# Kernel tuning notes

Hardware: AMD Instinct MI355X
Metric: run time of the kernel (lower is better)

The kernel has to match this reference:

```python
import jax, jax.numpy as jnp
import numpy as np

N, D = 8192, 128
T = 0.0025   # threshold t
M = 0.5      # margin m
K = 16
EPS = 1e-12


def _l2norm(x):
    return x / jnp.sqrt(jnp.sum(x * x, axis=-1, keepdims=True) + EPS)


def setup_inputs() -> dict:
    key = jax.random.key(0)
    k1, k2 = jax.random.split(key)
    yi = jax.random.normal(k1, (N, D), dtype=jnp.float32)
    yi_t = jax.random.normal(k2, (N, D), dtype=jnp.float32)
    return {"yi": yi, "yi_t": yi_t}


def reference(yi, yi_t):
    yin = _l2norm(yi)      # normalized yi, [N, D]
    yit = _l2norm(yi_t)    # normalized yi_t, [N, D]

    # pairwise L2 distances among normalized yi via norm expansion (avoids [N,N,D])
    sq = jnp.sum(yin * yin, axis=-1)                          # [N]
    d2 = sq[:, None] + sq[None, :] - 2.0 * (yin @ yin.T)      # [N, N]
    dis = jnp.sqrt(jnp.maximum(d2, 0.0) + EPS)

    # K+1 smallest distances per row (index 0 is self: self-dist = sqrt(EPS))
    _, idx = jax.lax.top_k(-dis, K + 1)                       # [N, K+1]

    yj = yin[idx[:, 1:]]    # [N, K, D] K nearest neighbors (excluding self)
    yij = yin[idx[:, 1]]    # [N, D]    nearest neighbor

    dis_yij = 0.5 * jnp.sqrt(jnp.sum((yin[:, None, :] - yj) ** 2, axis=-1) + EPS)   # [N, K]
    dis_yi_tj = 0.5 * jnp.sqrt(jnp.sum((yit[:, None, :] - yj) ** 2, axis=-1) + EPS)  # [N, K]

    out1 = (dis_yij - dis_yi_tj) ** 2 - T
    e1 = jnp.sum(jnp.where(out1 > 0, out1, 0.0))

    dis_yi_yi_t = 0.5 * jnp.sqrt(jnp.sum((yin - yit) ** 2, axis=-1) + EPS)  # [N]
    dis_yi_yij = 0.5 * jnp.sqrt(jnp.sum((yin - yij) ** 2, axis=-1) + EPS)   # [N]

    out2 = dis_yi_yi_t + M - dis_yi_yij
    e2 = jnp.sum(jnp.where(out2 > 0, out2, 0.0))

    return (e1 + e2, e1, e2)
```

## Files before the change

### kernel.cpp

```cpp
#include <hip/hip_runtime.h>
#include <hip/hip_bf16.h>
#include <math.h>


#define NPTS 8192
#define DIM 128
#define KNB 16
#define CAP 192
static constexpr float TAU = 0.20f;
static constexpr float T_THR = 0.0025f;
static constexpr float MARGIN = 0.5f;
static constexpr float EPSF = 1e-12f;

typedef __bf16 bf16x8 __attribute__((ext_vector_type(8)));
typedef float f32x4 __attribute__((ext_vector_type(4)));
struct bf2 { __bf16 x, y; };

__device__ __forceinline__ float bf2f(unsigned short u) {
    union { unsigned u32; float f; } c;
    c.u32 = ((unsigned)u) << 16;
    return c.f;
}

__global__ __launch_bounds__(256) void k_norm(const float* __restrict__ yi,
                                              const float* __restrict__ yit,
                                              __bf16* __restrict__ yb,
                                              __bf16* __restrict__ ybt,
                                              float* __restrict__ dyt,
                                              int* __restrict__ cnt) {
    const int g = blockIdx.x * 256 + threadIdx.x;
    if (g < NPTS) cnt[g] = 0;
    const int wid = threadIdx.x >> 6;
    const int lane = threadIdx.x & 63;
    const int row = blockIdx.x * 4 + wid;

    float2 v1 = *(const float2*)(yi + (size_t)row * DIM + lane * 2);
    float2 v2 = *(const float2*)(yit + (size_t)row * DIM + lane * 2);
    float s1 = v1.x * v1.x + v1.y * v1.y;
    float s2 = v2.x * v2.x + v2.y * v2.y;
    #pragma unroll
    for (int o = 32; o; o >>= 1) {
        s1 += __shfl_xor(s1, o);
        s2 += __shfl_xor(s2, o);
    }
    const float r1 = 1.0f / sqrtf(s1 + EPSF);
    const float r2 = 1.0f / sqrtf(s2 + EPSF);
    const float ax = v1.x * r1, ay = v1.y * r1;
    const float bx = v2.x * r2, by = v2.y * r2;
    bf2 oa{(__bf16)ax, (__bf16)ay};
    bf2 ob{(__bf16)bx, (__bf16)by};
    *(bf2*)(yb + (size_t)row * DIM + lane * 2) = oa;
    *(bf2*)(ybt + (size_t)row * DIM + lane * 2) = ob;

    float dd = (ax - bx) * (ax - bx) + (ay - by) * (ay - by);
    #pragma unroll
    for (int o = 32; o; o >>= 1) dd += __shfl_xor(dd, o);
    if (lane == 0) dyt[row] = 0.5f * sqrtf(dd + EPSF);
}

__global__ __launch_bounds__(256, 4) void k_screen(const __bf16* __restrict__ yb,
                                                   int* __restrict__ cnt,
                                                   unsigned* __restrict__ bucket) {
    __shared__ unsigned bucket_l[256 * 32];
    const int tid = threadIdx.x;
    const int wid = tid >> 6;
    const int lane = tid & 63;
    const int c15 = lane & 15;
    const int hi = lane >> 4;
    const int rb = blockIdx.x >> 5;
    const int cs = blockIdx.x & 31;
    const int wrow0 = rb * 256 + wid * 64;
    const int col0 = cs * 256;

    bf16x8 A[4][4];
    #pragma unroll
    for (int rt = 0; rt < 4; ++rt)
        #pragma unroll
        for (int t = 0; t < 4; ++t)
            A[rt][t] = *(const bf16x8*)(yb + (size_t)(wrow0 + rt * 16 + c15) * DIM + t * 32 + hi * 8);

    int cntr[4] = {0, 0, 0, 0};

    #pragma unroll 2
    for (int tile = 0; tile < 16; ++tile) {
        const int jc = col0 + tile * 16 + c15;
        const __bf16* bp = yb + (size_t)jc * DIM + hi * 8;
        const bf16x8 B0 = *(const bf16x8*)(bp);
        const bf16x8 B1 = *(const bf16x8*)(bp + 32);
        const bf16x8 B2 = *(const bf16x8*)(bp + 64);
        const bf16x8 B3 = *(const bf16x8*)(bp + 96);

        f32x4 acc[4];
        #pragma unroll
        for (int rt = 0; rt < 4; ++rt) {
            f32x4 z = {0.0f, 0.0f, 0.0f, 0.0f};
            acc[rt] = __builtin_amdgcn_mfma_f32_16x16x32_bf16(B0, A[rt][0], z, 0, 0, 0);
            acc[rt] = __builtin_amdgcn_mfma_f32_16x16x32_bf16(B1, A[rt][1], acc[rt], 0, 0, 0);
            acc[rt] = __builtin_amdgcn_mfma_f32_16x16x32_bf16(B2, A[rt][2], acc[rt], 0, 0, 0);
            acc[rt] = __builtin_amdgcn_mfma_f32_16x16x32_bf16(B3, A[rt][3], acc[rt], 0, 0, 0);
        }

        const int cb = col0 + tile * 16 + (hi << 2);
        const unsigned kbase = (unsigned)(8191 - cb);
        #pragma unroll
        for (int rt = 0; rt < 4; ++rt) {
            unsigned* bl = &bucket_l[(wid * 64 + rt * 16 + c15) * 32 + hi * 8];
            #pragma unroll
            for (int r = 0; r < 4; ++r) {
                const float v = acc[rt][r];
                const bool h = v > TAU;
                const unsigned key =
                    (__float_as_uint(v) & 0xFFFFE000u) | (kbase - (unsigned)r);
                const int idx = min(cntr[rt], 7);
                if (h) bl[idx] = key;
                cntr[rt] += (int)h;
            }
        }
    }

    unsigned cpack = (unsigned)min(cntr[0], 8) | ((unsigned)min(cntr[1], 8) << 8) |
                     ((unsigned)min(cntr[2], 8) << 16) | ((unsigned)min(cntr[3], 8) << 24);
    asm volatile("s_waitcnt lgkmcnt(0)" ::: "memory");
    {
        const int rt = (tid >> 4) & 3;
        const int cl = tid & 15;
        int c[4], total = 0;
        #pragma unroll
        for (int h2 = 0; h2 < 4; ++h2) {
            unsigned cp = __shfl(cpack, h2 * 16 + cl);
            c[h2] = (int)((cp >> (rt * 8)) & 255u);
            total += c[h2];
        }
        if (total > 0) {
            const int grow = rb * 256 + tid;
            int p = atomicAdd(&cnt[grow], total);
            const unsigned* bl = &bucket_l[tid * 32];
            #pragma unroll
            for (int h2 = 0; h2 < 4; ++h2)
                for (int s = 0; s < c[h2]; ++s) {
                    if (p < CAP) bucket[(size_t)grow * CAP + p] = bl[h2 * 8 + s];
                    ++p;
                }
        }
    }
}

__global__ __launch_bounds__(256) void k_selloss(const __bf16* __restrict__ yb,
                                                 const __bf16* __restrict__ ybt,
                                                 const int* __restrict__ cnt,
                                                 const unsigned* __restrict__ bucketK,
                                                 const float* __restrict__ dyt,
                                                 float* __restrict__ e1row,
                                                 float* __restrict__ e2row) {
    __shared__ unsigned nbrk[4][KNB];
    const int wid = threadIdx.x >> 6;
    const int lane = threadIdx.x & 63;
    const int row = blockIdx.x * 4 + wid;

    const int cn = min(cnt[row], CAP);
    unsigned val[3];
    #pragma unroll
    for (int s = 0; s < 3; ++s) {
        const int p = s * 64 + lane;
        val[s] = (p < cn) ? bucketK[(size_t)row * CAP + p] : 0u;
    }

    unsigned prefix = 0u;
    int need = 17;
    #pragma unroll 1
    for (int b = 29; b >= 0; --b) {
        const unsigned cand = prefix | (1u << b);
        int c = 0;
        #pragma unroll
        for (int s = 0; s < 3; ++s)
            c += __popcll(__ballot(((val[s] ^ cand) >> b) == 0u));
        if (c >= need) prefix = cand;
        else need -= c;
    }

    bool sel[3];
    unsigned m1 = 0u;
    #pragma unroll
    for (int s = 0; s < 3; ++s) {
        const int jj = 8191 - (int)(val[s] & 0x1FFFu);
        sel[s] = (val[s] >= prefix) && (jj != row);
        if (sel[s] && val[s] > m1) m1 = val[s];
    }
    #pragma unroll
    for (int o = 32; o; o >>= 1) {
        unsigned ov = __shfl_xor(m1, o);
        m1 = ov > m1 ? ov : m1;
    }
    {
        const unsigned long long b0 = __ballot(sel[0]);
        const unsigned long long b1 = __ballot(sel[1]);
        const unsigned long long b2 = __ballot(sel[2]);
        const unsigned long long lt = ((unsigned long long)1 << lane) - 1;
        const int n0 = __popcll(b0), n1 = __popcll(b1);
        const int p0 = __popcll(b0 & lt);
        const int p1 = n0 + __popcll(b1 & lt);
        const int p2 = n0 + n1 + __popcll(b2 & lt);
        if (sel[0] && p0 < KNB) nbrk[wid][p0] = val[0];
        if (sel[1] && p1 < KNB) nbrk[wid][p1] = val[1];
        if (sel[2] && p2 < KNB) nbrk[wid][p2] = val[2];
    }

    const int n = lane >> 2;
    const int cch = lane & 3;
    const unsigned key = nbrk[wid][n];
    const int j = (8191 - (int)(key & 0x1FFFu)) & (NPTS - 1);
    const bf16x8* pj = (const bf16x8*)(yb + (size_t)j * DIM + cch * 32);
    const bf16x8* pi = (const bf16x8*)(ybt + (size_t)row * DIM + cch * 32);
    float dd = 0.0f;
    #pragma unroll
    for (int q = 0; q < 4; ++q) {
        bf16x8 a = pi[q], b = pj[q];
        #pragma unroll
        for (int e = 0; e < 8; ++e) {
            const float d = bf2f(((const unsigned short*)&a)[e]) -
                            bf2f(((const unsigned short*)&b)[e]);
            dd += d * d;
        }
    }
    #pragma unroll
    for (int o = 1; o <= 2; o <<= 1) dd += __shfl_xor(dd, o);

    const float dotk = __uint_as_float(key & 0xFFFFE000u);
    const float da = 0.5f * sqrtf(fmaxf(2.0f - 2.0f * dotk, 0.0f) + EPSF);
    const float db = 0.5f * sqrtf(dd + EPSF);
    float o1 = (da - db) * (da - db) - T_THR;
    o1 = (cch == 0) ? fmaxf(o1, 0.0f) : 0.0f;
    #pragma unroll
    for (int o = 4; o <= 32; o <<= 1) o1 += __shfl_xor(o1, o);

    if (lane == 0) {
        const float dot1 = __uint_as_float(m1 & 0xFFFFE000u);
        const float d0 = 0.5f * sqrtf(fmaxf(2.0f - 2.0f * dot1, 0.0f) + EPSF);
        e1row[row] = o1;
        e2row[row] = fmaxf(dyt[row] + MARGIN - d0, 0.0f);
    }
}

__global__ __launch_bounds__(1024) void k_red(const float* __restrict__ e1row,
                                              const float* __restrict__ e2row,
                                              float* __restrict__ out) {
    __shared__ float s1[1024], s2[1024];
    float a = 0.0f, b = 0.0f;
    for (int i = threadIdx.x; i < NPTS; i += 1024) {
        a += e1row[i];
        b += e2row[i];
    }
    s1[threadIdx.x] = a;
    s2[threadIdx.x] = b;
    __syncthreads();
    for (int st = 512; st; st >>= 1) {
        if (threadIdx.x < st) {
            s1[threadIdx.x] += s1[threadIdx.x + st];
            s2[threadIdx.x] += s2[threadIdx.x + st];
        }
        __syncthreads();
    }
    if (threadIdx.x == 0) {
        float e1 = s1[0], e2 = s2[0];
        out[0] = e1 + e2;
        out[1] = e1;
        out[2] = e2;
    }
}

extern "C" void kernel_launch(void* const* d_in, const int* in_sizes, int n_in,
                              void* d_out, int out_size, void* d_ws, size_t ws_size,
                              hipStream_t stream) {
    const float* yi = (const float*)d_in[0];
    const float* yit = (const float*)d_in[1];

    __bf16* yb = (__bf16*)d_ws;
    __bf16* ybt = yb + (size_t)NPTS * DIM;
    int* cnt = (int*)(ybt + (size_t)NPTS * DIM);
    unsigned* bucketK = (unsigned*)(cnt + NPTS);
    float* dyt = (float*)(bucketK + (size_t)NPTS * CAP);
    float* e1row = dyt + NPTS;
    float* e2row = e1row + NPTS;

    k_norm<<<NPTS / 4, 256, 0, stream>>>(yi, yit, yb, ybt, dyt, cnt);
    k_screen<<<1024, 256, 0, stream>>>(yb, cnt, bucketK);
    k_selloss<<<NPTS / 4, 256, 0, stream>>>(yb, ybt, cnt, bucketK, dyt, e1row, e2row);
    k_red<<<1, 1024, 0, stream>>>(e1row, e2row, (float*)d_out);
}
```

Baseline: 68.43 us.

## Halve screen tile rows per block to raise occupancy and shrink LDS buckets

The screening kernel now gives each wave 32 rows instead of 64 and launches twice as many blocks. It cuts the per-lane LDS bucket slots from 8 to 6 and requests 8 waves per EU. MFMA chains for the two row tiles are interleaved so independent work sits between dependent steps. The goal is to lower register and LDS pressure so more waves can hide load latency. In exchange, each B column tile is reloaded twice as often, and rows with more than 6 hits per 16-column segment lose more candidates, which could change the kNN selection.

```diff
diff --git a/kernel.cpp b/kernel.cpp
--- a/kernel.cpp
+++ b/kernel.cpp
@@ -7,6 +7,7 @@
 #define DIM 128
 #define KNB 16
 #define CAP 192
+#define SLOTS 6
 static constexpr float TAU = 0.20f;
 static constexpr float T_THR = 0.0025f;
 static constexpr float MARGIN = 0.5f;
@@ -58,10 +59,12 @@
     if (lane == 0) dyt[row] = 0.5f * sqrtf(dd + EPSF);
 }
 
-__global__ __launch_bounds__(256, 4) void k_screen(const __bf16* __restrict__ yb,
-                                                   int* __restrict__ cnt,
-                                                   unsigned* __restrict__ bucket) {
-    __shared__ unsigned bucket_l[256 * 32];
+__global__ __launch_bounds__(256)
+__attribute__((amdgpu_waves_per_eu(8)))
+void k_screen(const __bf16* __restrict__ yb,
+              int* __restrict__ cnt,
+              unsigned* __restrict__ bucket) {
+    __shared__ unsigned bucket_l[128 * 4 * SLOTS];
     const int tid = threadIdx.x;
     const int wid = tid >> 6;
     const int lane = tid & 63;
@@ -69,17 +72,24 @@
     const int hi = lane >> 4;
     const int rb = blockIdx.x >> 5;
     const int cs = blockIdx.x & 31;
-    const int wrow0 = rb * 256 + wid * 64;
+    const int wrow0 = rb * 128 + wid * 32;
     const int col0 = cs * 256;
 
-    bf16x8 A[4][4];
-    #pragma unroll
-    for (int rt = 0; rt < 4; ++rt)
+    bf16x8 A[2][4];
+    #pragma unroll
+    for (int rt = 0; rt < 2; ++rt)
         #pragma unroll
         for (int t = 0; t < 4; ++t)
             A[rt][t] = *(const bf16x8*)(yb + (size_t)(wrow0 + rt * 16 + c15) * DIM + t * 32 + hi * 8);
-
-    int cntr[4] = {0, 0, 0, 0};
+    #pragma unroll
+    for (int rt = 0; rt < 2; ++rt)
+        #pragma unroll
+        for (int t = 0; t < 4; ++t)
+            asm volatile("" : "+v"(A[rt][t]));
+
+    int cntr0 = 0, cntr1 = 0;
+    unsigned* bl0 = &bucket_l[((wid * 32 + c15) * 4 + hi) * SLOTS];
+    unsigned* bl1 = &bucket_l[((wid * 32 + 16 + c15) * 4 + hi) * SLOTS];
 
     #pragma unroll 2
     for (int tile = 0; tile < 16; ++tile) {
@@ -90,40 +100,44 @@
         const bf16x8 B2 = *(const bf16x8*)(bp + 64);
         const bf16x8 B3 = *(const bf16x8*)(bp + 96);
 
-        f32x4 acc[4];
-        #pragma unroll
-        for (int rt = 0; rt < 4; ++rt) {
-            f32x4 z = {0.0f, 0.0f, 0.0f, 0.0f};
-            acc[rt] = __builtin_amdgcn_mfma_f32_16x16x32_bf16(B0, A[rt][0], z, 0, 0, 0);
-            acc[rt] = __builtin_amdgcn_mfma_f32_16x16x32_bf16(B1, A[rt][1], acc[rt], 0, 0, 0);
-            acc[rt] = __builtin_amdgcn_mfma_f32_16x16x32_bf16(B2, A[rt][2], acc[rt], 0, 0, 0);
-            acc[rt] = __builtin_amdgcn_mfma_f32_16x16x32_bf16(B3, A[rt][3], acc[rt], 0, 0, 0);
-        }
+        f32x4 z = {0.0f, 0.0f, 0.0f, 0.0f};
+        f32x4 a0, a1;
+        a0 = __builtin_amdgcn_mfma_f32_16x16x32_bf16(B0, A[0][0], z, 0, 0, 0);
+        a1 = __builtin_amdgcn_mfma_f32_16x16x32_bf16(B0, A[1][0], z, 0, 0, 0);
+        a0 = __builtin_amdgcn_mfma_f32_16x16x32_bf16(B1, A[0][1], a0, 0, 0, 0);
+        a1 = __builtin_amdgcn_mfma_f32_16x16x32_bf16(B1, A[1][1], a1, 0, 0, 0);
+        a0 = __builtin_amdgcn_mfma_f32_16x16x32_bf16(B2, A[0][2], a0, 0, 0, 0);
+        a1 = __builtin_amdgcn_mfma_f32_16x16x32_bf16(B2, A[1][2], a1, 0, 0, 0);
+        a0 = __builtin_amdgcn_mfma_f32_16x16x32_bf16(B3, A[0][3], a0, 0, 0, 0);
+        a1 = __builtin_amdgcn_mfma_f32_16x16x32_bf16(B3, A[1][3], a1, 0, 0, 0);
 
         const int cb = col0 + tile * 16 + (hi << 2);
         const unsigned kbase = (unsigned)(8191 - cb);
         #pragma unroll
-        for (int rt = 0; rt < 4; ++rt) {
-            unsigned* bl = &bucket_l[(wid * 64 + rt * 16 + c15) * 32 + hi * 8];
-            #pragma unroll
-            for (int r = 0; r < 4; ++r) {
-                const float v = acc[rt][r];
-                const bool h = v > TAU;
-                const unsigned key =
-                    (__float_as_uint(v) & 0xFFFFE000u) | (kbase - (unsigned)r);
-                const int idx = min(cntr[rt], 7);
-                if (h) bl[idx] = key;
-                cntr[rt] += (int)h;
-            }
-        }
-    }
-
-    unsigned cpack = (unsigned)min(cntr[0], 8) | ((unsigned)min(cntr[1], 8) << 8) |
-                     ((unsigned)min(cntr[2], 8) << 16) | ((unsigned)min(cntr[3], 8) << 24);
+        for (int r = 0; r < 4; ++r) {
+            const float v = a0[r];
+            const bool h = v > TAU;
+            const unsigned key = (__float_as_uint(v) & 0xFFFFE000u) | (kbase - (unsigned)r);
+            const int idx = min(cntr0, SLOTS - 1);
+            if (h) bl0[idx] = key;
+            cntr0 += (int)h;
+        }
+        #pragma unroll
+        for (int r = 0; r < 4; ++r) {
+            const float v = a1[r];
+            const bool h = v > TAU;
+            const unsigned key = (__float_as_uint(v) & 0xFFFFE000u) | (kbase - (unsigned)r);
+            const int idx = min(cntr1, SLOTS - 1);
+            if (h) bl1[idx] = key;
+            cntr1 += (int)h;
+        }
+    }
+
+    unsigned cpack = (unsigned)min(cntr0, SLOTS) | ((unsigned)min(cntr1, SLOTS) << 8);
     asm volatile("s_waitcnt lgkmcnt(0)" ::: "memory");
     {
-        const int rt = (tid >> 4) & 3;
-        const int cl = tid & 15;
+        const int rt = (lane >> 4) & 1;
+        const int cl = lane & 15;
         int c[4], total = 0;
         #pragma unroll
         for (int h2 = 0; h2 < 4; ++h2) {
@@ -131,14 +145,15 @@
             c[h2] = (int)((cp >> (rt * 8)) & 255u);
             total += c[h2];
         }
-        if (total > 0) {
-            const int grow = rb * 256 + tid;
+        if (lane < 32 && total > 0) {
+            const int rloc = wid * 32 + rt * 16 + cl;
+            const int grow = rb * 128 + rloc;
             int p = atomicAdd(&cnt[grow], total);
-            const unsigned* bl = &bucket_l[tid * 32];
+            const unsigned* bl = &bucket_l[rloc * 4 * SLOTS];
             #pragma unroll
             for (int h2 = 0; h2 < 4; ++h2)
                 for (int s = 0; s < c[h2]; ++s) {
-                    if (p < CAP) bucket[(size_t)grow * CAP + p] = bl[h2 * 8 + s];
+                    if (p < CAP) bucket[(size_t)grow * CAP + p] = bl[h2 * SLOTS + s];
                     ++p;
                 }
         }
@@ -283,7 +298,7 @@
     float* e2row = e1row + NPTS;
 
     k_norm<<<NPTS / 4, 256, 0, stream>>>(yi, yit, yb, ybt, dyt, cnt);
-    k_screen<<<1024, 256, 0, stream>>>(yb, cnt, bucketK);
+    k_screen<<<2048, 256, 0, stream>>>(yb, cnt, bucketK);
     k_selloss<<<NPTS / 4, 256, 0, stream>>>(yb, ybt, cnt, bucketK, dyt, e1row, e2row);
     k_red<<<1, 1024, 0, stream>>>(e1row, e2row, (float*)d_out);
 }
```

After: 112.3 us. +64.1%, slower.
